# Optimization experiments

Measured on AMD Instinct MI355X. Metric: run time of the kernel, lower is better.

The kernel has to match this reference:

```python
import jax, jax.numpy as jnp
import numpy as np

B, N, E, F, FE, H = 4, 1024, 65536, 96, 32, 12
DH = F // H
EPS = 1e-3  # keras LayerNormalization default epsilon


def layer_norm(x, g, b):
    m = jnp.mean(x, axis=-1, keepdims=True)
    v = jnp.var(x, axis=-1, keepdims=True)
    return (x - m) / jnp.sqrt(v + EPS) * g + b


def setup_inputs() -> dict:
    key = jax.random.key(0)
    ks = jax.random.split(key, 14)
    s = lambda d: 1.0 / np.sqrt(d)
    return {
        "nodes": jax.random.normal(ks[0], (B, N, F), jnp.float32),
        "edge_features": jax.random.normal(ks[1], (B, E, FE), jnp.float32),
        "distance": jax.random.uniform(ks[2], (B, E, 1), jnp.float32),
        "edges": jax.random.randint(ks[3], (B, E, 2), 0, N, jnp.int32),
        # message MLP: Dense(2F+FE -> F) + GELU + LayerNorm
        "Wm": jax.random.normal(ks[4], (2 * F + FE, F), jnp.float32) * s(2 * F + FE),
        "bm": jnp.zeros((F,), jnp.float32),
        "g1": jnp.ones((F,), jnp.float32),
        "b1": jnp.zeros((F,), jnp.float32),
        # gated multi-head self-attention over concat([nodes, aggregated]) (2F -> F)
        "Wq": jax.random.normal(ks[5], (2 * F, F), jnp.float32) * s(2 * F),
        "bq": jnp.zeros((F,), jnp.float32),
        "Wk": jax.random.normal(ks[6], (2 * F, F), jnp.float32) * s(2 * F),
        "bk": jnp.zeros((F,), jnp.float32),
        "Wv": jax.random.normal(ks[7], (2 * F, F), jnp.float32) * s(2 * F),
        "bv": jnp.zeros((F,), jnp.float32),
        "Wg": jax.random.normal(ks[8], (2 * F, F), jnp.float32) * s(2 * F),
        "bg": jnp.zeros((F,), jnp.float32),
        "Wo": jax.random.normal(ks[9], (F, F), jnp.float32) * s(F),
        "bo": jnp.zeros((F,), jnp.float32),
        "g2": jnp.ones((F,), jnp.float32),
        "b2": jnp.zeros((F,), jnp.float32),
        # learnable gaussian edge-weight params
        "sigma": jnp.full((1,), 0.005, jnp.float32),
        "beta": jnp.full((1,), 4.0, jnp.float32),
    }


def reference(nodes, edge_features, distance, edges, Wm, bm, g1, b1,
              Wq, bq, Wk, bk, Wv, bv, Wg, bg, Wo, bo, g2, b2, sigma, beta):
    # --- message: gather endpoint node features per edge ---
    gathered = jax.vmap(lambda n, e: n[e])(nodes, edges)              # [B,E,2,F]
    msg_in = jnp.concatenate([gathered.reshape(B, E, 2 * F), edge_features], axis=-1)
    messages = layer_norm(jax.nn.gelu(msg_in @ Wm + bm, approximate=False), g1, b1)  # [B,E,F]
    # --- learnable gaussian edge weighting ---
    edge_weights = jnp.exp(-((distance ** 2 / (2.0 * sigma ** 2)) ** beta))           # [B,E,1]
    weighted_messages = messages * edge_weights
    # --- scatter: per-graph segment-sum into receiver nodes (edge[:,1]) ---
    aggregated = jax.vmap(lambda m, seg: jax.ops.segment_sum(m, seg, num_segments=N))(
        weighted_messages, edges[..., 1])                             # [B,N,F]
    # --- update: gated multi-head self-attention on concat([nodes, aggregated]) ---
    x = jnp.concatenate([nodes, aggregated], axis=-1)                 # [B,N,2F]
    heads = lambda t: t.reshape(B, N, H, DH).transpose(0, 2, 1, 3)    # [B,H,N,DH]
    q, k, v = heads(x @ Wq + bq), heads(x @ Wk + bk), heads(x @ Wv + bv)
    gate = heads(jax.nn.sigmoid(x @ Wg + bg))
    attn = jax.nn.softmax(jnp.einsum("bhqd,bhkd->bhqk", q, k) / jnp.sqrt(jnp.float32(DH)), axis=-1)
    out = (jnp.einsum("bhqk,bhkd->bhqd", attn, v) * gate).transpose(0, 2, 1, 3).reshape(B, N, F)
    out = out @ Wo + bo
    updated_nodes = layer_norm(jax.nn.gelu(out, approximate=False), g2, b2)
    return (updated_nodes, weighted_messages, distance, edges)
```

## Files before the change

### kernel.cpp

```cpp
#include <hip/hip_runtime.h>
#include <math.h>

#define Bn 4
#define Nn 1024
#define En 65536
#define Fn 96
#define FEn 32
#define Hn 12

#define OUT_UPD  0
#define OUT_WM   393216LL
#define OUT_DIST 25559040LL
#define OUT_EDGE 25821184LL

#define WS_AGG  0
#define WS_Q    393216
#define WS_K    786432
#define WS_V    1179648
#define WS_G    1572864
#define WS_AO   1966080
#define WS_LIST 2359296
#define WS_LW   2424832
#define WS_CNT  2490368

#define MSG_NWAVES 1024

typedef __attribute__((ext_vector_type(8))) short bf16x8;
typedef __attribute__((ext_vector_type(4))) float f32x4;

__device__ __forceinline__ float gelu_exact(float x) {
    return 0.5f * x * (1.0f + erff(x * 0.70710678118654752f));
}

__device__ __forceinline__ unsigned cvtpk_bf16(float lo, float hi) {
    unsigned r;
    asm("v_cvt_pk_bf16_f32 %0, %1, %2" : "=v"(r) : "v"(lo), "v"(hi));
    return r;
}

__device__ __forceinline__ void zero_wm_chunk(int c, const float* __restrict__ dist,
                                              const float* __restrict__ sigma,
                                              const float* __restrict__ beta,
                                              float* __restrict__ out_wm,
                                              int tid, int nthr, int* s_act) {
    if (tid < 256) {
        int ge = c * 256 + tid;
        float d = dist[ge];
        float sg = sigma[0], bt = beta[0];
        float t = d * d / (2.0f * sg * sg);
        s_act[tid] = (powf(t, bt) < 90.0f) ? 1 : 0;
    }
    __syncthreads();
    const float4 z = make_float4(0.f, 0.f, 0.f, 0.f);
    float4* wm4 = (float4*)out_wm + (size_t)c * 6144;
    for (int p = tid; p < 6144; p += nthr) {
        if (!s_act[p / 24]) wm4[p] = z;
    }
}

__global__ void zero_kernel(float* __restrict__ agg, int* __restrict__ gcnt) {
    int i = blockIdx.x * 256 + threadIdx.x;
    const float4 z = make_float4(0.f, 0.f, 0.f, 0.f);
    float4* p = (float4*)agg;
    p[i] = z;
    p[i + 49152] = z;
    if (i == 0) gcnt[0] = 0;
}

__global__ __launch_bounds__(1024) void scan_kernel(
        const float* __restrict__ dist, const int* __restrict__ edges,
        const float* __restrict__ sigma, const float* __restrict__ beta,
        float* __restrict__ out_dist, float* __restrict__ out_edges,
        int* __restrict__ glist, float* __restrict__ gw,
        int* __restrict__ gcnt) {
    __shared__ int wcnt[16], wbase[16], blkbase;
    int tid = threadIdx.x;
    int lane = tid & 63, wv = tid >> 6;
    int ge = blockIdx.x * 1024 + tid;
    float d = dist[ge];
    out_dist[ge] = d;
    int e0 = edges[2 * ge], e1 = edges[2 * ge + 1];
    *(float2*)&out_edges[2 * ge] = make_float2((float)e0, (float)e1);
    float sg = sigma[0], bt = beta[0];
    float t  = d * d / (2.0f * sg * sg);
    float tp = powf(t, bt);
    bool active = (tp < 90.0f);
    float w = active ? expf(-tp) : 0.0f;

    unsigned long long mask = __ballot(active);
    int lp = __popcll(mask & ((1ull << lane) - 1ull));
    if (lane == 0) wcnt[wv] = __popcll(mask);
    __syncthreads();
    if (tid == 0) {
        int a = 0;
        #pragma unroll
        for (int i = 0; i < 16; ++i) { wbase[i] = a; a += wcnt[i]; }
        blkbase = a ? atomicAdd(gcnt, a) : 0;
    }
    __syncthreads();
    if (active) {
        int pos = blkbase + wbase[wv] + lp;
        if (pos < 65536) { glist[pos] = ge; gw[pos] = w; }
    }
}

__global__ __launch_bounds__(256) void msg_kernel(
        const int* __restrict__ glist, const float* __restrict__ gw,
        const int* __restrict__ gcnt, const int* __restrict__ edges,
        const float* __restrict__ nodes, const float* __restrict__ ef,
        const float* __restrict__ Wm, const float* __restrict__ bm,
        const float* __restrict__ g1, const float* __restrict__ b1,
        float* __restrict__ out_wm, float* __restrict__ agg) {
    __shared__ float sin_s[4][4][232];
    int tid = threadIdx.x;
    int lane = tid & 63, wv = tid >> 6;
    int count = gcnt[0];
    if (count > 65536) count = 65536;
    int c2 = 64 + (lane & 31);
    int wid = blockIdx.x * 4 + wv;

    for (int base = wid * 4; base < count; base += MSG_NWAVES * 4) {
        int   gei[4];
        float wgt[4];
        bool  val[4];
        #pragma unroll
        for (int e = 0; e < 4; ++e) {
            int ai = base + e;
            val[e] = (ai < count);
            int as = val[e] ? ai : base;
            gei[e] = glist[as];
            wgt[e] = val[e] ? gw[ai] : 0.0f;
        }
        #pragma unroll
        for (int e = 0; e < 4; ++e) {
            int g = gei[e];
            int b = g >> 16;
            int e0 = edges[2 * g], e1 = edges[2 * g + 1];
            const float* n0 = nodes + ((size_t)b * Nn + e0) * 96;
            const float* n1 = nodes + ((size_t)b * Nn + e1) * 96;
            const float* ep = ef + (size_t)g * 32;
            #pragma unroll
            for (int ii = 0; ii < 4; ++ii) {
                int i = ii * 64 + lane;
                if (i < 224) {
                    float v = (i < 96) ? n0[i] : (i < 192) ? n1[i - 96] : ep[i - 192];
                    sin_s[wv][e][i] = v;
                }
            }
        }
        float acc[4][2];
        #pragma unroll
        for (int e = 0; e < 4; ++e) { acc[e][0] = bm[lane]; acc[e][1] = bm[c2]; }
        #pragma unroll 8
        for (int i = 0; i < 224; ++i) {
            float w1 = Wm[i * 96 + lane];
            float w2 = Wm[i * 96 + c2];
            #pragma unroll
            for (int e = 0; e < 4; ++e) {
                float a = sin_s[wv][e][i];
                acc[e][0] = fmaf(a, w1, acc[e][0]);
                acc[e][1] = fmaf(a, w2, acc[e][1]);
            }
        }
        #pragma unroll
        for (int e = 0; e < 4; ++e) {
            if (!val[e]) continue;
            float y1 = gelu_exact(acc[e][0]);
            float y2 = gelu_exact(acc[e][1]);
            float c2v = (lane < 32) ? y2 : 0.0f;
            float sum  = y1 + c2v;
            float sum2 = y1 * y1 + c2v * c2v;
            #pragma unroll
            for (int off = 1; off < 64; off <<= 1) {
                sum  += __shfl_xor(sum, off);
                sum2 += __shfl_xor(sum2, off);
            }
            float mean = sum * (1.0f / 96.0f);
            float var  = sum2 * (1.0f / 96.0f) - mean * mean;
            float rs   = rsqrtf(var + 1e-3f);
            int g = gei[e];
            int b = g >> 16;
            int e1 = edges[2 * g + 1];
            float* aggp = agg + ((size_t)b * Nn + e1) * 96;
            float* wmp  = out_wm + (size_t)g * 96;
            float o1 = ((y1 - mean) * rs * g1[lane] + b1[lane]) * wgt[e];
            wmp[lane] = o1;
            atomicAdd(&aggp[lane], o1);
            if (lane < 32) {
                float o2 = ((y2 - mean) * rs * g1[c2] + b1[c2]) * wgt[e];
                wmp[c2] = o2;
                atomicAdd(&aggp[c2], o2);
            }
        }
    }
}

__global__ void proj_kernel(const float* __restrict__ nodes, const float* __restrict__ agg,
                            const float* __restrict__ Wq, const float* __restrict__ bq,
                            const float* __restrict__ Wk, const float* __restrict__ bk,
                            const float* __restrict__ Wv, const float* __restrict__ bv,
                            const float* __restrict__ Wg, const float* __restrict__ bg,
                            float* __restrict__ qo, float* __restrict__ ko,
                            float* __restrict__ vo, float* __restrict__ go,
                            const float* __restrict__ dist, const float* __restrict__ sigma,
                            const float* __restrict__ beta, float* __restrict__ out_wm) {
    __shared__ float xs[32][200];
    __shared__ float Wt[64 * 96];
    __shared__ int s_act[256];
    int tid = threadIdx.x;
    int m = blockIdx.y;
    if (m == 0) {
        zero_wm_chunk(768 + blockIdx.x, dist, sigma, beta, out_wm, tid, 256, s_act);
    }
    const float* W    = (m == 0) ? Wq : (m == 1) ? Wk : (m == 2) ? Wv : Wg;
    const float* bias = (m == 0) ? bq : (m == 1) ? bk : (m == 2) ? bv : bg;
    float* outp       = (m == 0) ? qo : (m == 1) ? ko : (m == 2) ? vo : go;
    int row0 = blockIdx.x * 32;
    int b = row0 >> 10, n0 = row0 & 1023;
    for (int i = tid; i < 32 * 192; i += 256) {
        int r = i / 192, k = i % 192;
        size_t row = row0 + r;
        xs[r][k] = (k < 96) ? nodes[row * 96 + k] : agg[row * 96 + (k - 96)];
    }
    int rg = tid >> 4;
    int cg = tid & 15;
    float acc[12];
    #pragma unroll
    for (int c = 0; c < 12; ++c) acc[c] = 0.0f;
    for (int kc = 0; kc < 3; ++kc) {
        __syncthreads();
        {
            float4* Wt4 = (float4*)Wt;
            const float4* Wg4 = (const float4*)(W + kc * 64 * 96);
            for (int i = tid; i < 1536; i += 256) Wt4[i] = Wg4[i];
        }
        __syncthreads();
        #pragma unroll 4
        for (int k = 0; k < 64; ++k) {
            float a0 = xs[rg * 2 + 0][kc * 64 + k];
            float a1 = xs[rg * 2 + 1][kc * 64 + k];
            #pragma unroll
            for (int c = 0; c < 6; ++c) {
                float wv_ = Wt[k * 96 + cg * 6 + c];
                acc[c]     = fmaf(a0, wv_, acc[c]);
                acc[6 + c] = fmaf(a1, wv_, acc[6 + c]);
            }
        }
    }
    #pragma unroll
    for (int i = 0; i < 2; ++i) {
        #pragma unroll
        for (int c = 0; c < 6; ++c) {
            int col = cg * 6 + c;
            float v = acc[i * 6 + c] + bias[col];
            if (m == 3) v = 1.0f / (1.0f + expf(-v));
            xs[rg * 2 + i][col] = v;
        }
    }
    __syncthreads();
    float4* out4 = (float4*)outp;
    for (int j = tid; j < 768; j += 256) {
        int h = j >> 6, idx = j & 63;
        int r = idx >> 1, half = idx & 1;
        float4 v = *(const float4*)&xs[r][h * 8 + half * 4];
        out4[(((size_t)b * Hn + h) * Nn + n0) * 2 + idx] = v;
    }
}

__global__ __launch_bounds__(256, 4) void attn_kernel(
        const float* __restrict__ qp, const float* __restrict__ kp,
        const float* __restrict__ vp, const float* __restrict__ gp,
        float* __restrict__ ao,
        const float* __restrict__ dist, const float* __restrict__ sigma,
        const float* __restrict__ beta, float* __restrict__ out_wm) {
    __shared__ __align__(16) unsigned short K_s[1024][8];
    __shared__ __align__(16) unsigned short Vt_s[9][1032];
    __shared__ __align__(16) unsigned short P_s[4][16][32];
    __shared__ int s_act[256];
    int tid = threadIdx.x;
    zero_wm_chunk(blockIdx.y * 16 + blockIdx.x, dist, sigma, beta, out_wm, tid, 256, s_act);

    int bh = blockIdx.y;
    int lane = tid & 63, wv = tid >> 6;
    size_t hb = (size_t)bh * (Nn * 8);
    const float* kc = kp + hb;
    const float* vc = vp + hb;

    {
        const float2* k2 = (const float2*)kc;
        unsigned* kw = (unsigned*)&K_s[0][0];
        for (int i = tid; i < 4096; i += 256) {
            float2 v = k2[i];
            kw[i] = cvtpk_bf16(v.x, v.y);
        }
    }
    for (int i = tid; i < 8192; i += 256) {
        float v = vc[i];
        int k = i >> 3, n = i & 7;
        Vt_s[n][k] = (unsigned short)cvtpk_bf16(v, v);
    }
    {
        unsigned* ow = (unsigned*)&Vt_s[8][0];
        for (int i = tid; i < 516; i += 256) ow[i] = 0x3F803F80u;
    }

    const float scale = 0.35355339059327376f;
    int qbase = blockIdx.x * 64 + wv * 16;
    bf16x8 aq = {0, 0, 0, 0, 0, 0, 0, 0};
    if (lane < 16) {
        const float* qr = qp + hb + (size_t)(qbase + lane) * 8;
        float4 qa = *(const float4*)qr;
        float4 qb2 = *(const float4*)(qr + 4);
        union { unsigned u[4]; bf16x8 v; } U;
        U.u[0] = cvtpk_bf16(qa.x * scale, qa.y * scale);
        U.u[1] = cvtpk_bf16(qa.z * scale, qa.w * scale);
        U.u[2] = cvtpk_bf16(qb2.x * scale, qb2.y * scale);
        U.u[3] = cvtpk_bf16(qb2.z * scale, qb2.w * scale);
        aq = U.v;
    }
    __syncthreads();

    const bf16x8 zero8 = {0, 0, 0, 0, 0, 0, 0, 0};
    const f32x4 zero4 = {0.f, 0.f, 0.f, 0.f};
    f32x4 o = zero4;
    int n16 = lane & 15, grp = lane >> 4;
    for (int c = 0; c < 32; ++c) {
        bf16x8 bk0 = zero8, bk1 = zero8;
        if (lane < 16) {
            bk0 = *(const bf16x8*)&K_s[c * 32 + lane][0];
            bk1 = *(const bf16x8*)&K_s[c * 32 + 16 + lane][0];
        }
        f32x4 s0 = __builtin_amdgcn_mfma_f32_16x16x32_bf16(aq, bk0, zero4, 0, 0, 0);
        f32x4 s1 = __builtin_amdgcn_mfma_f32_16x16x32_bf16(aq, bk1, zero4, 0, 0, 0);
        #pragma unroll
        for (int r = 0; r < 4; ++r) {
            unsigned pk = cvtpk_bf16(__expf(s0[r]), __expf(s1[r]));
            int row = grp * 4 + r;
            P_s[wv][row][n16]      = (unsigned short)pk;
            P_s[wv][row][16 + n16] = (unsigned short)(pk >> 16);
        }
        bf16x8 pa = *(const bf16x8*)&P_s[wv][n16][grp * 8];
        bf16x8 bv = zero8;
        if (n16 <= 8) bv = *(const bf16x8*)&Vt_s[n16][c * 32 + grp * 8];
        o = __builtin_amdgcn_mfma_f32_16x16x32_bf16(pa, bv, o, 0, 0, 0);
    }

    #pragma unroll
    for (int r = 0; r < 4; ++r) {
        float L = __shfl(o[r], (lane & 48) | 8);
        if (n16 < 8) {
            int q = qbase + grp * 4 + r;
            size_t off = hb + (size_t)q * 8 + n16;
            ao[off] = o[r] / L * gp[off];
        }
    }
}

__global__ __launch_bounds__(512) void out_kernel(
        const float* __restrict__ ao, const float* __restrict__ Wo,
        const float* __restrict__ bo, const float* __restrict__ g2,
        const float* __restrict__ b2, float* __restrict__ out0,
        const float* __restrict__ dist, const float* __restrict__ sigma,
        const float* __restrict__ beta, float* __restrict__ out_wm) {
    __shared__ float Wsh[96 * 96];
    __shared__ float as_[32][104];
    __shared__ int s_act[256];
    int tid = threadIdx.x;
    zero_wm_chunk(896 + blockIdx.x, dist, sigma, beta, out_wm, tid, 512, s_act);
    int row0 = blockIdx.x * 32;
    int b = row0 >> 10, n0 = row0 & 1023;
    {
        float4* W4 = (float4*)Wsh;
        const float4* Wg4 = (const float4*)Wo;
        for (int i = tid; i < 2304; i += 512) W4[i] = Wg4[i];
    }
    const float4* ao4 = (const float4*)ao;
    for (int j = tid; j < 768; j += 512) {
        int h = j >> 6, idx = j & 63;
        int r = idx >> 1, half = idx & 1;
        float4 v = ao4[(((size_t)b * Hn + h) * Nn + n0) * 2 + idx];
        *(float4*)&as_[r][h * 8 + half * 4] = v;
    }
    __syncthreads();
    int r = tid >> 4, cg = tid & 15;
    float acc[6];
    #pragma unroll
    for (int c = 0; c < 6; ++c) acc[c] = 0.0f;
    for (int k = 0; k < 96; ++k) {
        float a = as_[r][k];
        #pragma unroll
        for (int c = 0; c < 6; ++c)
            acc[c] = fmaf(a, Wsh[k * 96 + cg * 6 + c], acc[c]);
    }
    float yv[6];
    float sum = 0.0f, sum2 = 0.0f;
    #pragma unroll
    for (int c = 0; c < 6; ++c) {
        float t = acc[c] + bo[cg * 6 + c];
        float g = gelu_exact(t);
        yv[c] = g;
        sum += g; sum2 += g * g;
    }
    #pragma unroll
    for (int off = 1; off < 16; off <<= 1) {
        sum  += __shfl_xor(sum, off);
        sum2 += __shfl_xor(sum2, off);
    }
    float mean = sum * (1.0f / 96.0f);
    float var  = sum2 * (1.0f / 96.0f) - mean * mean;
    float rs   = rsqrtf(var + 1e-3f);
    size_t row = row0 + r;
    #pragma unroll
    for (int c = 0; c < 6; ++c)
        out0[row * 96 + cg * 6 + c] = (yv[c] - mean) * rs * g2[cg * 6 + c] + b2[cg * 6 + c];
}

extern "C" void kernel_launch(void* const* d_in, const int* in_sizes, int n_in,
                              void* d_out, int out_size, void* d_ws, size_t ws_size,
                              hipStream_t stream) {
    const float* nodes = (const float*)d_in[0];
    const float* ef    = (const float*)d_in[1];
    const float* dist  = (const float*)d_in[2];
    const int*   edges = (const int*)d_in[3];
    const float* Wm = (const float*)d_in[4];
    const float* bm = (const float*)d_in[5];
    const float* g1 = (const float*)d_in[6];
    const float* b1 = (const float*)d_in[7];
    const float* Wq = (const float*)d_in[8];
    const float* bq = (const float*)d_in[9];
    const float* Wk = (const float*)d_in[10];
    const float* bk = (const float*)d_in[11];
    const float* Wv = (const float*)d_in[12];
    const float* bv = (const float*)d_in[13];
    const float* Wg = (const float*)d_in[14];
    const float* bg = (const float*)d_in[15];
    const float* Wo = (const float*)d_in[16];
    const float* bo = (const float*)d_in[17];
    const float* g2 = (const float*)d_in[18];
    const float* b2 = (const float*)d_in[19];
    const float* sigma = (const float*)d_in[20];
    const float* beta  = (const float*)d_in[21];

    float* out = (float*)d_out;
    float* ws  = (float*)d_ws;

    float* agg  = ws + WS_AGG;
    float* qb   = ws + WS_Q;
    float* kb   = ws + WS_K;
    float* vb   = ws + WS_V;
    float* gwb  = ws + WS_G;
    float* aob  = ws + WS_AO;
    int*   glist = (int*)(ws + WS_LIST);
    float* glw   = ws + WS_LW;
    int*   gcnt  = (int*)(ws + WS_CNT);

    zero_kernel<<<192, 256, 0, stream>>>(agg, gcnt);

    scan_kernel<<<Bn * En / 1024, 1024, 0, stream>>>(
        dist, edges, sigma, beta, out + OUT_DIST, out + OUT_EDGE, glist, glw, gcnt);

    msg_kernel<<<256, 256, 0, stream>>>(
        glist, glw, gcnt, edges, nodes, ef, Wm, bm, g1, b1, out + OUT_WM, agg);

    dim3 gp_(128, 4);
    proj_kernel<<<gp_, 256, 0, stream>>>(
        nodes, agg, Wq, bq, Wk, bk, Wv, bv, Wg, bg, qb, kb, vb, gwb,
        dist, sigma, beta, out + OUT_WM);

    dim3 ga(16, Bn * Hn);
    attn_kernel<<<ga, 256, 0, stream>>>(qb, kb, vb, gwb, aob,
                                        dist, sigma, beta, out + OUT_WM);

    out_kernel<<<Bn * Nn / 32, 512, 0, stream>>>(aob, Wo, bo, g2, b2, out + OUT_UPD,
                                                 dist, sigma, beta, out + OUT_WM);
}
```

Before: 112.2 us.

## Stage Wm in LDS, restructure proj/out GEMMs per-wave column tiles, rebalance zeroing

The message kernel now loads the full 224x96 Wm matrix into shared memory once per block and reads weights from there instead of global memory. It also uses fewer blocks, and blocks with no work exit early. The projection and output kernels are restructured so each wave owns a column slice and each lane owns a row. Weights are read through scalar/uniform global loads, activations are stored transposed in LDS, and outputs are written as float4. The zeroing of weighted-message chunks is moved out of the output kernel and spread across all four projection blocks. The LDS footprint of msg_kernel grows to about 100KB, which limits occupancy, and the output kernel's LayerNorm now needs an extra cross-wave LDS reduction.

```diff
diff --git a/kernel.cpp b/kernel.cpp
--- a/kernel.cpp
+++ b/kernel.cpp
@@ -23,7 +23,8 @@
 #define WS_LW   2424832
 #define WS_CNT  2490368
 
-#define MSG_NWAVES 1024
+#define MSG_BLOCKS 208
+#define MSG_NWAVES (MSG_BLOCKS * 4)
 
 typedef __attribute__((ext_vector_type(8))) short bf16x8;
 typedef __attribute__((ext_vector_type(4))) float f32x4;
@@ -111,11 +112,19 @@
         const float* __restrict__ Wm, const float* __restrict__ bm,
         const float* __restrict__ g1, const float* __restrict__ b1,
         float* __restrict__ out_wm, float* __restrict__ agg) {
+    __shared__ float Wm_s[224 * 96];
     __shared__ float sin_s[4][4][232];
     int tid = threadIdx.x;
-    int lane = tid & 63, wv = tid >> 6;
     int count = gcnt[0];
     if (count > 65536) count = 65536;
+    if ((int)blockIdx.x * 16 >= count) return;
+    {
+        float4* Ws4 = (float4*)Wm_s;
+        const float4* Wg4 = (const float4*)Wm;
+        for (int i = tid; i < 5376; i += 256) Ws4[i] = Wg4[i];
+    }
+    __syncthreads();
+    int lane = tid & 63, wv = tid >> 6;
     int c2 = 64 + (lane & 31);
     int wid = blockIdx.x * 4 + wv;
 
@@ -153,8 +162,8 @@
         for (int e = 0; e < 4; ++e) { acc[e][0] = bm[lane]; acc[e][1] = bm[c2]; }
         #pragma unroll 8
         for (int i = 0; i < 224; ++i) {
-            float w1 = Wm[i * 96 + lane];
-            float w2 = Wm[i * 96 + c2];
+            float w1 = Wm_s[i * 96 + lane];
+            float w2 = Wm_s[i * 96 + c2];
             #pragma unroll
             for (int e = 0; e < 4; ++e) {
                 float a = sin_s[wv][e][i];
@@ -195,75 +204,59 @@
     }
 }
 
-__global__ void proj_kernel(const float* __restrict__ nodes, const float* __restrict__ agg,
-                            const float* __restrict__ Wq, const float* __restrict__ bq,
-                            const float* __restrict__ Wk, const float* __restrict__ bk,
-                            const float* __restrict__ Wv, const float* __restrict__ bv,
-                            const float* __restrict__ Wg, const float* __restrict__ bg,
-                            float* __restrict__ qo, float* __restrict__ ko,
-                            float* __restrict__ vo, float* __restrict__ go,
-                            const float* __restrict__ dist, const float* __restrict__ sigma,
-                            const float* __restrict__ beta, float* __restrict__ out_wm) {
-    __shared__ float xs[32][200];
-    __shared__ float Wt[64 * 96];
+__global__ __launch_bounds__(256) void proj_kernel(
+        const float* __restrict__ nodes, const float* __restrict__ agg,
+        const float* __restrict__ Wq, const float* __restrict__ bq,
+        const float* __restrict__ Wk, const float* __restrict__ bk,
+        const float* __restrict__ Wv, const float* __restrict__ bv,
+        const float* __restrict__ Wg, const float* __restrict__ bg,
+        float* __restrict__ qo, float* __restrict__ ko,
+        float* __restrict__ vo, float* __restrict__ go,
+        const float* __restrict__ dist, const float* __restrict__ sigma,
+        const float* __restrict__ beta, float* __restrict__ out_wm) {
+    __shared__ float xs[192][65];
     __shared__ int s_act[256];
     int tid = threadIdx.x;
     int m = blockIdx.y;
-    if (m == 0) {
-        zero_wm_chunk(768 + blockIdx.x, dist, sigma, beta, out_wm, tid, 256, s_act);
-    }
+    zero_wm_chunk(768 + m * 64 + blockIdx.x, dist, sigma, beta, out_wm, tid, 256, s_act);
+
     const float* W    = (m == 0) ? Wq : (m == 1) ? Wk : (m == 2) ? Wv : Wg;
     const float* bias = (m == 0) ? bq : (m == 1) ? bk : (m == 2) ? bv : bg;
     float* outp       = (m == 0) ? qo : (m == 1) ? ko : (m == 2) ? vo : go;
-    int row0 = blockIdx.x * 32;
+    int row0 = blockIdx.x * 64;
     int b = row0 >> 10, n0 = row0 & 1023;
-    for (int i = tid; i < 32 * 192; i += 256) {
+
+    for (int i = tid; i < 64 * 192; i += 256) {
         int r = i / 192, k = i % 192;
-        size_t row = row0 + r;
-        xs[r][k] = (k < 96) ? nodes[row * 96 + k] : agg[row * 96 + (k - 96)];
-    }
-    int rg = tid >> 4;
-    int cg = tid & 15;
-    float acc[12];
-    #pragma unroll
-    for (int c = 0; c < 12; ++c) acc[c] = 0.0f;
-    for (int kc = 0; kc < 3; ++kc) {
-        __syncthreads();
-        {
-            float4* Wt4 = (float4*)Wt;
-            const float4* Wg4 = (const float4*)(W + kc * 64 * 96);
-            for (int i = tid; i < 1536; i += 256) Wt4[i] = Wg4[i];
-        }
-        __syncthreads();
-        #pragma unroll 4
-        for (int k = 0; k < 64; ++k) {
-            float a0 = xs[rg * 2 + 0][kc * 64 + k];
-            float a1 = xs[rg * 2 + 1][kc * 64 + k];
-            #pragma unroll
-            for (int c = 0; c < 6; ++c) {
-                float wv_ = Wt[k * 96 + cg * 6 + c];
-                acc[c]     = fmaf(a0, wv_, acc[c]);
-                acc[6 + c] = fmaf(a1, wv_, acc[6 + c]);
-            }
-        }
-    }
-    #pragma unroll
-    for (int i = 0; i < 2; ++i) {
-        #pragma unroll
-        for (int c = 0; c < 6; ++c) {
-            int col = cg * 6 + c;
-            float v = acc[i * 6 + c] + bias[col];
-            if (m == 3) v = 1.0f / (1.0f + expf(-v));
-            xs[rg * 2 + i][col] = v;
-        }
-    }
-    __syncthreads();
+        size_t row = (size_t)row0 + r;
+        xs[k][r] = (k < 96) ? nodes[row * 96 + k] : agg[row * 96 + (k - 96)];
+    }
+    __syncthreads();
+
+    int lane = tid & 63;
+    int wcol = __builtin_amdgcn_readfirstlane((tid >> 6) * 24);
+    const float* Wp = W + wcol;
+    const float* bp = bias + wcol;
+    float acc[24];
+    #pragma unroll
+    for (int c = 0; c < 24; ++c) acc[c] = bp[c];
+    for (int k = 0; k < 192; ++k) {
+        float a = xs[k][lane];
+        #pragma unroll
+        for (int c = 0; c < 24; ++c)
+            acc[c] = fmaf(a, Wp[k * 96 + c], acc[c]);
+    }
+    if (m == 3) {
+        #pragma unroll
+        for (int c = 0; c < 24; ++c) acc[c] = 1.0f / (1.0f + expf(-acc[c]));
+    }
     float4* out4 = (float4*)outp;
-    for (int j = tid; j < 768; j += 256) {
-        int h = j >> 6, idx = j & 63;
-        int r = idx >> 1, half = idx & 1;
-        float4 v = *(const float4*)&xs[r][h * 8 + half * 4];
-        out4[(((size_t)b * Hn + h) * Nn + n0) * 2 + idx] = v;
+    int h0 = wcol >> 3;
+    #pragma unroll
+    for (int hh = 0; hh < 3; ++hh) {
+        size_t base = (((size_t)b * Hn + (h0 + hh)) * Nn + (n0 + lane)) * 2;
+        out4[base]     = make_float4(acc[hh*8+0], acc[hh*8+1], acc[hh*8+2], acc[hh*8+3]);
+        out4[base + 1] = make_float4(acc[hh*8+4], acc[hh*8+5], acc[hh*8+6], acc[hh*8+7]);
     }
 }
 
@@ -303,7 +296,6 @@
         unsigned* ow = (unsigned*)&Vt_s[8][0];
         for (int i = tid; i < 516; i += 256) ow[i] = 0x3F803F80u;
     }
-
     const float scale = 0.35355339059327376f;
     int qbase = blockIdx.x * 64 + wv * 16;
     bf16x8 aq = {0, 0, 0, 0, 0, 0, 0, 0};
@@ -359,60 +351,57 @@
 __global__ __launch_bounds__(512) void out_kernel(
         const float* __restrict__ ao, const float* __restrict__ Wo,
         const float* __restrict__ bo, const float* __restrict__ g2,
-        const float* __restrict__ b2, float* __restrict__ out0,
-        const float* __restrict__ dist, const float* __restrict__ sigma,
-        const float* __restrict__ beta, float* __restrict__ out_wm) {
-    __shared__ float Wsh[96 * 96];
-    __shared__ float as_[32][104];
-    __shared__ int s_act[256];
+        const float* __restrict__ b2, float* __restrict__ out0) {
+    __shared__ float as_[96][65];
+    __shared__ float2 red_s[8][64];
     int tid = threadIdx.x;
-    zero_wm_chunk(896 + blockIdx.x, dist, sigma, beta, out_wm, tid, 512, s_act);
-    int row0 = blockIdx.x * 32;
+    int row0 = blockIdx.x * 64;
     int b = row0 >> 10, n0 = row0 & 1023;
-    {
-        float4* W4 = (float4*)Wsh;
-        const float4* Wg4 = (const float4*)Wo;
-        for (int i = tid; i < 2304; i += 512) W4[i] = Wg4[i];
-    }
     const float4* ao4 = (const float4*)ao;
-    for (int j = tid; j < 768; j += 512) {
-        int h = j >> 6, idx = j & 63;
-        int r = idx >> 1, half = idx & 1;
-        float4 v = ao4[(((size_t)b * Hn + h) * Nn + n0) * 2 + idx];
-        *(float4*)&as_[r][h * 8 + half * 4] = v;
-    }
-    __syncthreads();
-    int r = tid >> 4, cg = tid & 15;
-    float acc[6];
-    #pragma unroll
-    for (int c = 0; c < 6; ++c) acc[c] = 0.0f;
+    for (int j = tid; j < 1536; j += 512) {
+        int h = j >> 7, rem = j & 127, n = rem >> 1, half = rem & 1;
+        float4 v = ao4[(((size_t)b * Hn + h) * Nn + (n0 + n)) * 2 + half];
+        int kb = h * 8 + half * 4;
+        as_[kb + 0][n] = v.x; as_[kb + 1][n] = v.y;
+        as_[kb + 2][n] = v.z; as_[kb + 3][n] = v.w;
+    }
+    __syncthreads();
+    int lane = tid & 63, w = tid >> 6;
+    int wcol = __builtin_amdgcn_readfirstlane(w * 12);
+    const float* Wp = Wo + wcol;
+    float acc[12];
+    #pragma unroll
+    for (int c = 0; c < 12; ++c) acc[c] = 0.0f;
     for (int k = 0; k < 96; ++k) {
-        float a = as_[r][k];
-        #pragma unroll
-        for (int c = 0; c < 6; ++c)
-            acc[c] = fmaf(a, Wsh[k * 96 + cg * 6 + c], acc[c]);
-    }
-    float yv[6];
+        float a = as_[k][lane];
+        #pragma unroll
+        for (int c = 0; c < 12; ++c)
+            acc[c] = fmaf(a, Wp[k * 96 + c], acc[c]);
+    }
+    float y[12];
     float sum = 0.0f, sum2 = 0.0f;
     #pragma unroll
-    for (int c = 0; c < 6; ++c) {
-        float t = acc[c] + bo[cg * 6 + c];
+    for (int c = 0; c < 12; ++c) {
+        float t = acc[c] + bo[wcol + c];
         float g = gelu_exact(t);
-        yv[c] = g;
-        sum += g; sum2 += g * g;
-    }
-    #pragma unroll
-    for (int off = 1; off < 16; off <<= 1) {
-        sum  += __shfl_xor(sum, off);
-        sum2 += __shfl_xor(sum2, off);
-    }
-    float mean = sum * (1.0f / 96.0f);
-    float var  = sum2 * (1.0f / 96.0f) - mean * mean;
+        y[c] = g; sum += g; sum2 += g * g;
+    }
+    red_s[w][lane] = make_float2(sum, sum2);
+    __syncthreads();
+    float S = 0.0f, S2 = 0.0f;
+    #pragma unroll
+    for (int i = 0; i < 8; ++i) { float2 p = red_s[i][lane]; S += p.x; S2 += p.y; }
+    float mean = S * (1.0f / 96.0f);
+    float var  = S2 * (1.0f / 96.0f) - mean * mean;
     float rs   = rsqrtf(var + 1e-3f);
-    size_t row = row0 + r;
-    #pragma unroll
-    for (int c = 0; c < 6; ++c)
-        out0[row * 96 + cg * 6 + c] = (yv[c] - mean) * rs * g2[cg * 6 + c] + b2[cg * 6 + c];
+    size_t row = (size_t)row0 + lane;
+    #pragma unroll
+    for (int c = 0; c < 12; ++c)
+        y[c] = (y[c] - mean) * rs * g2[wcol + c] + b2[wcol + c];
+    float4* o4 = (float4*)&out0[row * 96 + wcol];
+    o4[0] = make_float4(y[0], y[1], y[2],  y[3]);
+    o4[1] = make_float4(y[4], y[5], y[6],  y[7]);
+    o4[2] = make_float4(y[8], y[9], y[10], y[11]);
 }
 
 extern "C" void kernel_launch(void* const* d_in, const int* in_sizes, int n_in,
@@ -459,10 +448,10 @@
     scan_kernel<<<Bn * En / 1024, 1024, 0, stream>>>(
         dist, edges, sigma, beta, out + OUT_DIST, out + OUT_EDGE, glist, glw, gcnt);
 
-    msg_kernel<<<256, 256, 0, stream>>>(
+    msg_kernel<<<MSG_BLOCKS, 256, 0, stream>>>(
         glist, glw, gcnt, edges, nodes, ef, Wm, bm, g1, b1, out + OUT_WM, agg);
 
-    dim3 gp_(128, 4);
+    dim3 gp_(64, 4);
     proj_kernel<<<gp_, 256, 0, stream>>>(
         nodes, agg, Wq, bq, Wk, bk, Wv, bv, Wg, bg, qb, kb, vb, gwb,
         dist, sigma, beta, out + OUT_WM);
@@ -471,6 +460,5 @@
     attn_kernel<<<ga, 256, 0, stream>>>(qb, kb, vb, gwb, aob,
                                         dist, sigma, beta, out + OUT_WM);
 
-    out_kernel<<<Bn * Nn / 32, 512, 0, stream>>>(aob, Wo, bo, g2, b2, out + OUT_UPD,
-                                                 dist, sigma, beta, out + OUT_WM);
-}
+    out_kernel<<<Bn * Nn / 64, 512, 0, stream>>>(aob, Wo, bo, g2, b2, out + OUT_UPD);
+}
```

After: 130.7 us. 1.17x slower.
